# Performance work log

Measured on AMD Instinct MI355X. Metric: run time of the kernel, lower is better.

## Reference

```python
import jax, jax.numpy as jnp
import numpy as np

EPS = 1e-5

def _instance_norm(t):
    # torch .var(dim=2) default is unbiased (ddof=1) over flattened HW
    b, c, h, w = t.shape
    flat = t.reshape(b, c, h * w)
    mean = flat.mean(axis=2)
    var = flat.var(axis=2, ddof=1) + EPS
    return (t - mean[:, :, None, None]) / jnp.sqrt(var)[:, :, None, None]

def _conv1x1(t, w, b):
    # w: [Cout, Cin], b: [Cout]; t: [B, Cin, H, W]
    return jnp.einsum('oc,bchw->bohw', w, t) + b[None, :, None, None]


def setup_inputs() -> dict:
    key = jax.random.key(0)
    ks = jax.random.split(key, 11)
    B, C, H, W = 4, 512, 64, 64
    scale = 1.0 / np.sqrt(C)
    inp = {
        'c': jax.random.normal(ks[0], (B, C, H, W), jnp.float32),
        's': jax.random.normal(ks[1], (B, C, H, W), jnp.float32),
        'x': jax.random.normal(ks[2], (B, C, H, W), jnp.float32),
        'c_w': jax.random.normal(ks[3], (C, C), jnp.float32) * scale,
        'c_b': jax.random.normal(ks[4], (C,), jnp.float32) * 0.01,
        's_w': jax.random.normal(ks[5], (C, C), jnp.float32) * scale,
        's_b': jax.random.normal(ks[6], (C,), jnp.float32) * 0.01,
        'i_w': jax.random.normal(ks[7], (C, C), jnp.float32) * scale,
        'i_b': jax.random.normal(ks[8], (C,), jnp.float32) * 0.01,
        'o_w': jax.random.normal(ks[9], (C, C), jnp.float32) * scale,
        'o_b': jax.random.normal(ks[10], (C,), jnp.float32) * 0.01,
    }
    return inp


def reference(c, s, x, c_w, c_b, s_w, s_b, i_w, i_b, o_w, o_b):
    B, C, H, W = c.shape
    N = H * W
    cf = _conv1x1(_instance_norm(c), c_w, c_b).reshape(B, C, N)
    sf = _conv1x1(_instance_norm(s), s_w, s_b).reshape(B, C, N)
    xf = _conv1x1(s, i_w, i_b).reshape(B, C, N)
    # mask[b, n, m] = sum_c cf[b, c, n] * sf[b, c, m]; softmax over m
    mask = jax.nn.softmax(jnp.einsum('bcn,bcm->bnm', cf, sf), axis=-1)
    # of = xf @ mask^T : of[b, c, n] = sum_m xf[b, c, m] * mask[b, n, m]
    of = jnp.einsum('bcm,bnm->bcn', xf, mask).reshape(B, C, H, W)
    of = _conv1x1(of, o_w, o_b)
    return x + of
```

## Files before the change

kernel.cpp:

```cpp
#include <hip/hip_runtime.h>

typedef unsigned short u16;
typedef _Float16 f16x8 __attribute__((ext_vector_type(8)));
typedef float f32x4 __attribute__((ext_vector_type(4)));
typedef u16 u16x4 __attribute__((ext_vector_type(4)));
typedef u16 u16x8v __attribute__((ext_vector_type(8)));

__device__ __forceinline__ u16 f2h(float f) {
    _Float16 h = (_Float16)f;
    return __builtin_bit_cast(u16, h);
}
__device__ __forceinline__ float h2f(u16 u) {
    return (float)__builtin_bit_cast(_Float16, u);
}

__global__ void __launch_bounds__(256) stats_kernel(
    const float* __restrict__ c, const float* __restrict__ s,
    float* __restrict__ mC, float* __restrict__ rC,
    float* __restrict__ mS, float* __restrict__ rS)
{
    const float* src = (blockIdx.y ? s : c) + (size_t)blockIdx.x * 4096;
    int t = threadIdx.x, lane = t & 63, wv = t >> 6;
    const float4* p = (const float4*)src;
    float sum = 0.f, sq = 0.f;
#pragma unroll
    for (int i = 0; i < 4; ++i) {
        float4 v = p[t + 256 * i];
        sum += v.x + v.y + v.z + v.w;
        sq  += v.x * v.x + v.y * v.y + v.z * v.z + v.w * v.w;
    }
#pragma unroll
    for (int m = 1; m < 64; m <<= 1) {
        sum += __shfl_xor(sum, m);
        sq  += __shfl_xor(sq, m);
    }
    __shared__ float sa[4], sb[4];
    if (!lane) { sa[wv] = sum; sb[wv] = sq; }
    __syncthreads();
    if (t == 0) {
        float S = sa[0] + sa[1] + sa[2] + sa[3];
        float Q = sb[0] + sb[1] + sb[2] + sb[3];
        float mean = S * (1.0f / 4096.0f);
        float var = (Q - 4096.0f * mean * mean) * (1.0f / 4095.0f);
        float rstd = rsqrtf(var + 1e-5f);
        if (blockIdx.y) { mS[blockIdx.x] = mean; rS[blockIdx.x] = rstd; }
        else            { mC[blockIdx.x] = mean; rC[blockIdx.x] = rstd; }
    }
}

__global__ void __launch_bounds__(256) packall(
    const float* __restrict__ c, const float* __restrict__ s,
    const float* __restrict__ mC, const float* __restrict__ rC,
    const float* __restrict__ mS, const float* __restrict__ rS,
    u16* __restrict__ cnT, u16* __restrict__ snT, u16* __restrict__ sRT)
{
    __shared__ float tile[32][33];
    int z = blockIdx.z;
    bool isS = z >= 4;
    int b = isS ? z - 4 : z;
    const float* src  = isS ? s : c;
    const float* mean = isS ? mS : mC;
    const float* rstd = isS ? rS : rC;
    u16* dh = isS ? snT : cnT;
    int n0 = blockIdx.x * 32, c0 = blockIdx.y * 32;
    int tx = threadIdx.x, ty = threadIdx.y;
    const float* sbp = src + ((size_t)b * 512 + c0) * 4096 + n0;
#pragma unroll
    for (int it = 0; it < 4; ++it) {
        int cc = ty + it * 8;
        tile[cc][tx] = sbp[(size_t)cc * 4096 + tx];
    }
    __syncthreads();
    int ch = c0 + tx;
    float mn = mean[b * 512 + ch];
    float rs = rstd[b * 512 + ch];
    size_t obase = ((size_t)b * 4096 + n0) * 512 + c0;
#pragma unroll
    for (int it = 0; it < 4; ++it) {
        int r = ty + it * 8;
        float v = tile[tx][r];
        size_t o = obase + (size_t)r * 512 + tx;
        dh[o] = f2h((v - mn) * rs);
        if (isS) sRT[o] = f2h(v);
    }
}

__global__ void __launch_bounds__(256) prep_kernel(
    const float* __restrict__ c_w, const float* __restrict__ s_w,
    const float* __restrict__ i_w, const float* __restrict__ o_w,
    u16* __restrict__ cwT, u16* __restrict__ swT,
    u16* __restrict__ iwT, u16* __restrict__ ow)
{
    int z = blockIdx.z;
    int tx = threadIdx.x, ty = threadIdx.y;
    if (z == 3) {
        size_t base = ((size_t)(blockIdx.y * 16 + blockIdx.x) * 256 +
                       (ty * 32 + tx)) * 4;
        float4 v = *(const float4*)(o_w + base);
        u16x4 o;
        o[0] = f2h(v.x); o[1] = f2h(v.y); o[2] = f2h(v.z); o[3] = f2h(v.w);
        *(u16x4*)(ow + base) = o;
        return;
    }
    const float* w = (z == 0) ? c_w : (z == 1) ? s_w : i_w;
    u16* wT = (z == 0) ? cwT : (z == 1) ? swT : iwT;
    __shared__ float tile[32][33];
    int c0 = blockIdx.x * 32, k0 = blockIdx.y * 32;
#pragma unroll
    for (int it = 0; it < 4; ++it) {
        int kk = ty + it * 8;
        tile[kk][tx] = w[(size_t)(k0 + kk) * 512 + c0 + tx];
    }
    __syncthreads();
#pragma unroll
    for (int it = 0; it < 4; ++it) {
        int r = ty + it * 8;
        wT[(size_t)(c0 + r) * 512 + k0 + tx] = f2h(tile[tx][r]);
    }
}

__global__ void __launch_bounds__(256) bias_prep(
    const float* __restrict__ o_w, const float* __restrict__ i_b,
    const float* __restrict__ o_b, const float* __restrict__ s_w,
    const float* __restrict__ c_b, float* __restrict__ v,
    float* __restrict__ wu)
{
    __shared__ float buf[512];
    int t = threadIdx.x;
    bool isWu = blockIdx.x >= 2;
    const float* vec = isWu ? c_b : i_b;
    buf[t] = vec[t]; buf[t + 256] = vec[t + 256];
    __syncthreads();
    int o = (blockIdx.x & 1) * 256 + t;
    if (!isWu) {
        float acc = o_b[o];
        const float* row = o_w + (size_t)o * 512;
        for (int k = 0; k < 512; ++k) acc += row[k] * buf[k];
        v[o] = acc;
    } else {
        float acc = 0.f;
        for (int k = 0; k < 512; ++k) acc += buf[k] * s_w[(size_t)k * 512 + o];
        wu[o] = acc;
    }
}

__global__ void __launch_bounds__(256) rowdot_kernel(
    const u16* __restrict__ snT, const float* __restrict__ wu,
    float* __restrict__ u)
{
    __shared__ float swu[512];
    int t = threadIdx.x;
    swu[t] = wu[t]; swu[t + 256] = wu[t + 256];
    __syncthreads();
    int lane = t & 63, wv = t >> 6;
    int row = blockIdx.x * 4 + wv;
    u16x8v h = *(const u16x8v*)(snT + (size_t)row * 512 + lane * 8);
    float acc = 0.f;
#pragma unroll
    for (int i = 0; i < 8; ++i) acc += h2f(h[i]) * swu[lane * 8 + i];
#pragma unroll
    for (int m = 1; m < 64; m <<= 1) acc += __shfl_xor(acc, m);
    if (!lane) u[row] = acc;
}

#define EPI_F32       0
#define EPI_PLAIN_F16 2

__device__ __forceinline__ void stageA(
    const u16* __restrict__ g, int ldk, int i0, int k0, char* tile, int wv, int lane)
{
#pragma unroll
    for (int cc = 0; cc < 4; ++cc) {
        int chunk = (wv * 4 + cc) * 64 + lane;
        int row  = chunk >> 3;
        int slot = chunk & 7;
        int gc   = slot ^ (row & 7);
        const u16* gp = g + (size_t)(i0 + row) * ldk + (k0 + gc * 8);
        char* lp = tile + (size_t)(wv * 4 + cc) * 1024;
        __builtin_amdgcn_global_load_lds(
            (const __attribute__((address_space(1))) unsigned int*)gp,
            (__attribute__((address_space(3))) unsigned int*)lp, 16, 0, 0);
    }
}
__device__ __forceinline__ void stageB(
    const u16* __restrict__ g, int ldk, int j0, int k0, char* tile, int wv, int lane)
{
#pragma unroll
    for (int cc = 0; cc < 2; ++cc) {
        int chunk = (wv * 2 + cc) * 64 + lane;
        int row  = chunk >> 3;
        int slot = chunk & 7;
        int gc   = slot ^ (row & 7);
        const u16* gp = g + (size_t)(j0 + row) * ldk + (k0 + gc * 8);
        char* lp = tile + (size_t)(wv * 2 + cc) * 1024;
        __builtin_amdgcn_global_load_lds(
            (const __attribute__((address_space(1))) unsigned int*)gp,
            (__attribute__((address_space(3))) unsigned int*)lp, 16, 0, 0);
    }
}

template<int EPI>
__global__ void __launch_bounds__(512) gemm_bt(
    const u16* __restrict__ A_, const u16* __restrict__ B_,
    int K, int ldk, const float* __restrict__ bias,
    const float* __restrict__ jb, long jbZ,
    float* __restrict__ outF_, u16* __restrict__ outH_,
    int ldo, int zdiv,
    long aBatch, long aChunk, long bBatch, long bChunk, long oZ)
{
    __shared__ char smem[49152];

    int bz = blockIdx.z;
    int batch = bz / zdiv, chunk = bz % zdiv;
    const u16* A  = A_ + (size_t)batch * aBatch + (size_t)chunk * aChunk;
    const u16* Bm = B_ + (size_t)batch * bBatch + (size_t)chunk * bChunk;

    int i0 = blockIdx.y * 256, j0 = blockIdx.x * 128;
    int tid = threadIdx.x, lane = tid & 63, wv = tid >> 6;
    int wr = wv >> 1, wc = wv & 1;
    int r15 = lane & 15, h4 = lane >> 4;

    f32x4 zero = {0.f, 0.f, 0.f, 0.f};
    f32x4 acc[4][4];
#pragma unroll
    for (int m = 0; m < 4; ++m)
#pragma unroll
        for (int n = 0; n < 4; ++n) acc[m][n] = zero;

    for (int k0 = 0; k0 < K; k0 += 64) {
        stageA(A, ldk, i0, k0, smem, wv, lane);
        stageB(Bm, ldk, j0, k0, smem + 32768, wv, lane);
        asm volatile("s_waitcnt vmcnt(0)" ::: "memory");
        __syncthreads();
#pragma unroll
        for (int ks = 0; ks < 2; ++ks) {
            f16x8 a[4], b[4];
#pragma unroll
            for (int m = 0; m < 4; ++m) {
                int row = wr * 64 + m * 16 + r15;
                int off = row * 128 + (((ks * 4 + h4) ^ (row & 7)) << 4);
                a[m] = *(const f16x8*)(smem + off);
            }
#pragma unroll
            for (int n = 0; n < 4; ++n) {
                int col = wc * 64 + n * 16 + r15;
                int off = col * 128 + (((ks * 4 + h4) ^ (col & 7)) << 4);
                b[n] = *(const f16x8*)(smem + 32768 + off);
            }
#pragma unroll
            for (int m = 0; m < 4; ++m)
#pragma unroll
                for (int n = 0; n < 4; ++n)
                    acc[m][n] = __builtin_amdgcn_mfma_f32_16x16x32_f16(a[m], b[n], acc[m][n], 0, 0, 0);
        }
        __syncthreads();
    }

    float* outF = outF_ ? outF_ + (size_t)bz * oZ : nullptr;
    u16* outH = outH_ ? outH_ + (size_t)bz * oZ : nullptr;
    const float* jbp = jb ? jb + (size_t)bz * jbZ : nullptr;

#pragma unroll
    for (int m = 0; m < 4; ++m)
#pragma unroll
        for (int n = 0; n < 4; ++n) {
            int ibase = i0 + wr * 64 + m * 16 + h4 * 4;
            int j = j0 + wc * 64 + n * 16 + r15;
#pragma unroll
            for (int r = 0; r < 4; ++r) {
                int i = ibase + r;
                float v = acc[m][n][r];
                if constexpr (EPI == EPI_PLAIN_F16) {
                    if (bias) v += bias[i];
                    if (jbp) v += jbp[j];
                    outH[(size_t)i * ldo + j] = f2h(v);
                } else {
                    outF[(size_t)i * ldo + j] = v;
                }
            }
        }
}

__device__ __forceinline__ void stage256(
    const u16* __restrict__ g, int r0, int k0, char* tile, int wv, int lane)
{
#pragma unroll
    for (int cc = 0; cc < 4; ++cc) {
        int grp = cc * 8 + wv;
        int chunk = grp * 64 + lane;
        int row  = chunk >> 3;
        int slot = chunk & 7;
        int gc   = slot ^ (row & 7);
        const u16* gp = g + (size_t)(r0 + row) * 512 + (k0 + gc * 8);
        char* lp = tile + (size_t)grp * 1024;
        __builtin_amdgcn_global_load_lds(
            (const __attribute__((address_space(1))) unsigned int*)gp,
            (__attribute__((address_space(3))) unsigned int*)lp, 16, 0, 0);
    }
}

__global__ void __launch_bounds__(512) glogits256(
    const u16* __restrict__ A_, const u16* __restrict__ B_,
    const float* __restrict__ jb_, u16* __restrict__ outH_,
    long aZ, long bZ, long jbZ, long oZ)
{
    extern __shared__ char smem[];

    int bz = blockIdx.z;
    const u16* A  = A_ + (size_t)bz * aZ;
    const u16* Bm = B_ + (size_t)bz * bZ;

    int i0 = blockIdx.y * 256, j0 = blockIdx.x * 256;
    int tid = threadIdx.x, lane = tid & 63, wv = tid >> 6;
    int wr = wv >> 2, wc = wv & 3;
    int r15 = lane & 15, h4 = lane >> 4;

    f32x4 zero = {0.f, 0.f, 0.f, 0.f};
    f32x4 acc[8][4];
#pragma unroll
    for (int m = 0; m < 8; ++m)
#pragma unroll
        for (int n = 0; n < 4; ++n) acc[m][n] = zero;

    for (int k0 = 0; k0 < 512; k0 += 64) {
        stage256(A,  i0, k0, smem,         wv, lane);
        stage256(Bm, j0, k0, smem + 32768, wv, lane);
        asm volatile("s_waitcnt vmcnt(0)" ::: "memory");
        __syncthreads();
#pragma unroll
        for (int ks = 0; ks < 2; ++ks) {
            f16x8 a[8], b[4];
#pragma unroll
            for (int m = 0; m < 8; ++m) {
                int row = wr * 128 + m * 16 + r15;
                int off = row * 128 + (((ks * 4 + h4) ^ (row & 7)) << 4);
                a[m] = *(const f16x8*)(smem + off);
            }
#pragma unroll
            for (int n = 0; n < 4; ++n) {
                int col = wc * 64 + n * 16 + r15;
                int off = col * 128 + (((ks * 4 + h4) ^ (col & 7)) << 4);
                b[n] = *(const f16x8*)(smem + 32768 + off);
            }
#pragma unroll
            for (int m = 0; m < 8; ++m)
#pragma unroll
                for (int n = 0; n < 4; ++n)
                    acc[m][n] = __builtin_amdgcn_mfma_f32_16x16x32_f16(a[m], b[n], acc[m][n], 0, 0, 0);
        }
        __syncthreads();
    }

    u16* outH = outH_ + (size_t)bz * oZ;
    const float* jbp = jb_ + (size_t)bz * jbZ;
#pragma unroll
    for (int m = 0; m < 8; ++m)
#pragma unroll
        for (int n = 0; n < 4; ++n) {
            int ibase = i0 + wr * 128 + m * 16 + h4 * 4;
            int j = j0 + wc * 64 + n * 16 + r15;
            float ub = jbp[j];
#pragma unroll
            for (int r = 0; r < 4; ++r) {
                int i = ibase + r;
                outH[(size_t)i * 4096 + j] = f2h(acc[m][n][r] + ub);
            }
        }
}

__global__ void __launch_bounds__(256) softmax16(u16* __restrict__ LP)
{
    u16x8v* row = (u16x8v*)(LP + (size_t)blockIdx.x * 4096);
    int t = threadIdx.x, lane = t & 63, wv = t >> 6;
    u16x8v ca = row[t], cb = row[t + 256];
    float va[8], vb[8];
    float mx = -3.4e38f;
#pragma unroll
    for (int i = 0; i < 8; ++i) {
        va[i] = h2f(ca[i]); vb[i] = h2f(cb[i]);
        mx = fmaxf(mx, fmaxf(va[i], vb[i]));
    }
#pragma unroll
    for (int m = 1; m < 64; m <<= 1) mx = fmaxf(mx, __shfl_xor(mx, m));
    __shared__ float sM[4], sS[4];
    if (!lane) sM[wv] = mx;
    __syncthreads();
    mx = fmaxf(fmaxf(sM[0], sM[1]), fmaxf(sM[2], sM[3]));
    float sum = 0.f;
#pragma unroll
    for (int i = 0; i < 8; ++i) {
        va[i] = __expf(va[i] - mx);
        vb[i] = __expf(vb[i] - mx);
        sum += va[i] + vb[i];
    }
#pragma unroll
    for (int m = 1; m < 64; m <<= 1) sum += __shfl_xor(sum, m);
    if (!lane) sS[wv] = sum;
    __syncthreads();
    sum = sS[0] + sS[1] + sS[2] + sS[3];
    float inv = 1.0f / sum;
    u16x8v oa, ob;
#pragma unroll
    for (int i = 0; i < 8; ++i) {
        oa[i] = f2h(va[i] * inv);
        ob[i] = f2h(vb[i] * inv);
    }
    row[t] = oa; row[t + 256] = ob;
}

__global__ void __launch_bounds__(256) reduce4resid(
    const u16* __restrict__ part, const float* __restrict__ xr,
    const float* __restrict__ v, float* __restrict__ out)
{
    const size_t PLANE = 2097152;
    int b = blockIdx.y;
    size_t g8 = ((size_t)blockIdx.x * 256 + threadIdx.x) * 8;
    const u16* p0 = part + (size_t)b * 4 * PLANE + g8;
    float acc[8] = {0.f, 0.f, 0.f, 0.f, 0.f, 0.f, 0.f, 0.f};
#pragma unroll
    for (int k = 0; k < 4; ++k) {
        u16x8v h = *(const u16x8v*)(p0 + (size_t)k * PLANE);
#pragma unroll
        for (int i = 0; i < 8; ++i) acc[i] += h2f(h[i]);
    }
    const float4* xv = (const float4*)(xr + (size_t)b * PLANE + g8);
    float4 x0 = xv[0], x1 = xv[1];
    float vc = v[g8 >> 12];
    float4 o0, o1;
    o0.x = acc[0] + x0.x + vc; o0.y = acc[1] + x0.y + vc;
    o0.z = acc[2] + x0.z + vc; o0.w = acc[3] + x0.w + vc;
    o1.x = acc[4] + x1.x + vc; o1.y = acc[5] + x1.y + vc;
    o1.z = acc[6] + x1.z + vc; o1.w = acc[7] + x1.w + vc;
    float4* op = (float4*)(out + (size_t)b * PLANE + g8);
    op[0] = o0; op[1] = o1;
}

extern "C" void kernel_launch(void* const* d_in, const int* in_sizes, int n_in,
                              void* d_out, int out_size, void* d_ws, size_t ws_size,
                              hipStream_t stream)
{
    const float* c   = (const float*)d_in[0];
    const float* s   = (const float*)d_in[1];
    const float* x   = (const float*)d_in[2];
    const float* c_w = (const float*)d_in[3];
    const float* c_b = (const float*)d_in[4];
    const float* s_w = (const float*)d_in[5];
    const float* s_b = (const float*)d_in[6];
    const float* i_w = (const float*)d_in[7];
    const float* i_b = (const float*)d_in[8];
    const float* o_w = (const float*)d_in[9];
    const float* o_b = (const float*)d_in[10];
    float* out = (float*)d_out;
    char* ws = (char*)d_ws;

    const int B = 4, C = 512, N = 4096;
    const size_t NC = (size_t)N * C;
    const size_t W2 = (size_t)C * C;
    const size_t NN = (size_t)N * N;
    const int SMEM256 = 65536;

    size_t off = 0;
    auto alloc = [&](size_t bytes) { size_t o = off; off += (bytes + 255) & ~(size_t)255; return o; };

    size_t o_meanC = alloc((size_t)B * C * 4);
    size_t o_rstdC = alloc((size_t)B * C * 4);
    size_t o_meanS = alloc((size_t)B * C * 4);
    size_t o_rstdS = alloc((size_t)B * C * 4);
    size_t o_cwT = alloc(W2 * 2);
    size_t o_swT = alloc(W2 * 2);
    size_t o_iwT = alloc(W2 * 2);
    size_t o_ow  = alloc(W2 * 2);
    size_t o_G   = alloc(W2 * 2);
    size_t o_W   = alloc(W2 * 2);
    size_t o_v   = alloc((size_t)C * 4);
    size_t o_wu  = alloc((size_t)C * 4);
    size_t o_u   = alloc((size_t)B * N * 4);
    size_t o_cnT = alloc(B * NC * 2);
    size_t o_snT = alloc(B * NC * 2);
    size_t o_sRT = alloc(B * NC * 2);
    size_t o_sgT = alloc(B * NC * 2);
    size_t o_sW  = alloc(B * NC * 2);
    size_t o_P   = alloc(2 * NN * 2);
    size_t o_pt  = alloc(8 * NC * 2);

    if (ws_size < off) {
        (void)hipMemsetAsync(d_out, 0, (size_t)out_size * 4, stream);
        return;
    }

    float* meanC = (float*)(ws + o_meanC);
    float* rstdC = (float*)(ws + o_rstdC);
    float* meanS = (float*)(ws + o_meanS);
    float* rstdS = (float*)(ws + o_rstdS);
    u16* cwT = (u16*)(ws + o_cwT);
    u16* swT = (u16*)(ws + o_swT);
    u16* iwT = (u16*)(ws + o_iwT);
    u16* ow  = (u16*)(ws + o_ow);
    u16* Gf  = (u16*)(ws + o_G);
    u16* Wf  = (u16*)(ws + o_W);
    float* vb = (float*)(ws + o_v);
    float* wu = (float*)(ws + o_wu);
    float* ub = (float*)(ws + o_u);
    u16* cnT = (u16*)(ws + o_cnT);
    u16* snT = (u16*)(ws + o_snT);
    u16* sRT = (u16*)(ws + o_sRT);
    u16* sgT = (u16*)(ws + o_sgT);
    u16* sW  = (u16*)(ws + o_sW);
    u16* Pb  = (u16*)(ws + o_P);
    u16* partH = (u16*)(ws + o_pt);

    stats_kernel<<<dim3(B * C, 2), 256, 0, stream>>>(c, s, meanC, rstdC, meanS, rstdS);
    packall<<<dim3(N / 32, C / 32, 8), dim3(32, 8), 0, stream>>>(
        c, s, meanC, rstdC, meanS, rstdS, cnT, snT, sRT);
    prep_kernel<<<dim3(16, 16, 4), dim3(32, 8), 0, stream>>>(
        c_w, s_w, i_w, o_w, cwT, swT, iwT, ow);
    bias_prep<<<dim3(4), 256, 0, stream>>>(o_w, i_b, o_b, s_w, c_b, vb, wu);
    gemm_bt<EPI_PLAIN_F16><<<dim3(4, 2, 2), 512, 0, stream>>>(
        cwT, swT, 512, 512, nullptr, nullptr, 0, nullptr, Gf, 512, 1,
        (long)(3 * W2), 0, (long)W2, 0, (long)W2);
    gemm_bt<EPI_PLAIN_F16><<<dim3(4, 16, B), 512, 0, stream>>>(
        snT, Gf, 512, 512, nullptr, nullptr, 0, nullptr, sgT, 512, 1,
        (long)NC, 0, 0, 0, (long)NC);
    gemm_bt<EPI_PLAIN_F16><<<dim3(32, 2, B), 512, 0, stream>>>(
        Wf, sRT, 512, 512, nullptr, nullptr, 0, nullptr, sW, 4096, 1,
        0, 0, (long)NC, 0, (long)NC);
    rowdot_kernel<<<dim3(B * N / 4), 256, 0, stream>>>(snT, wu, ub);
    for (int pb0 = 0; pb0 < B; pb0 += 2) {
        glogits256<<<dim3(16, 16, 2), 512, SMEM256, stream>>>(
            cnT + (size_t)pb0 * NC, sgT + (size_t)pb0 * NC,
            ub + (size_t)pb0 * N, Pb,
            (long)NC, (long)NC, (long)N, (long)NN);
        softmax16<<<dim3(2 * N), 256, 0, stream>>>(Pb);
        gemm_bt<EPI_PLAIN_F16><<<dim3(32, 2, 8), 512, 0, stream>>>(
            sW + (size_t)pb0 * NC, Pb, 1024, 4096, nullptr, nullptr, 0,
            nullptr, partH, 4096, 4,
            (long)NC, 1024L, (long)NN, 1024L, (long)NC);
        reduce4resid<<<dim3((int)(NC / 2048), 2), 256, 0, stream>>>(
            partH, x + (size_t)pb0 * NC, vb, out + (size_t)pb0 * NC);
    }
}
```

Measured before the change: 339.8 us.

## Fold instance-norm into the G matrix and fuse stats into the transpose pack

The separate stats pass over c and s is removed. Per-tile partial sums are now computed inside the transpose/pack kernel and reduced by a small statreduce kernel, and c and s are packed raw to f16 instead of normalized. The normalization is moved algebraically into a per-batch scaled G matrix (rC·G·rS) and a per-batch bias vector for the rowdot term, which also removes the duplicate sRT buffer. This saves one full read of c and s plus one f16 write, at the cost of extra small kernels and per-batch G copies. Dropping the mean subtraction on c should cancel under softmax, but relying on an unnormalized f16 path and E[x²]-mean² variance risks some precision loss.

```diff
diff --git a/kernel.cpp b/kernel.cpp
--- a/kernel.cpp
+++ b/kernel.cpp
@@ -14,54 +14,17 @@
     return (float)__builtin_bit_cast(_Float16, u);
 }
 
-__global__ void __launch_bounds__(256) stats_kernel(
+__global__ void __launch_bounds__(256) packstat(
     const float* __restrict__ c, const float* __restrict__ s,
-    float* __restrict__ mC, float* __restrict__ rC,
-    float* __restrict__ mS, float* __restrict__ rS)
-{
-    const float* src = (blockIdx.y ? s : c) + (size_t)blockIdx.x * 4096;
-    int t = threadIdx.x, lane = t & 63, wv = t >> 6;
-    const float4* p = (const float4*)src;
-    float sum = 0.f, sq = 0.f;
-#pragma unroll
-    for (int i = 0; i < 4; ++i) {
-        float4 v = p[t + 256 * i];
-        sum += v.x + v.y + v.z + v.w;
-        sq  += v.x * v.x + v.y * v.y + v.z * v.z + v.w * v.w;
-    }
-#pragma unroll
-    for (int m = 1; m < 64; m <<= 1) {
-        sum += __shfl_xor(sum, m);
-        sq  += __shfl_xor(sq, m);
-    }
-    __shared__ float sa[4], sb[4];
-    if (!lane) { sa[wv] = sum; sb[wv] = sq; }
-    __syncthreads();
-    if (t == 0) {
-        float S = sa[0] + sa[1] + sa[2] + sa[3];
-        float Q = sb[0] + sb[1] + sb[2] + sb[3];
-        float mean = S * (1.0f / 4096.0f);
-        float var = (Q - 4096.0f * mean * mean) * (1.0f / 4095.0f);
-        float rstd = rsqrtf(var + 1e-5f);
-        if (blockIdx.y) { mS[blockIdx.x] = mean; rS[blockIdx.x] = rstd; }
-        else            { mC[blockIdx.x] = mean; rC[blockIdx.x] = rstd; }
-    }
-}
-
-__global__ void __launch_bounds__(256) packall(
-    const float* __restrict__ c, const float* __restrict__ s,
-    const float* __restrict__ mC, const float* __restrict__ rC,
-    const float* __restrict__ mS, const float* __restrict__ rS,
-    u16* __restrict__ cnT, u16* __restrict__ snT, u16* __restrict__ sRT)
+    u16* __restrict__ cT, u16* __restrict__ sT,
+    float* __restrict__ pS, float* __restrict__ pQ)
 {
     __shared__ float tile[32][33];
     int z = blockIdx.z;
     bool isS = z >= 4;
-    int b = isS ? z - 4 : z;
-    const float* src  = isS ? s : c;
-    const float* mean = isS ? mS : mC;
-    const float* rstd = isS ? rS : rC;
-    u16* dh = isS ? snT : cnT;
+    int b = z & 3;
+    const float* src = isS ? s : c;
+    u16* dst = isS ? sT : cT;
     int n0 = blockIdx.x * 32, c0 = blockIdx.y * 32;
     int tx = threadIdx.x, ty = threadIdx.y;
     const float* sbp = src + ((size_t)b * 512 + c0) * 4096 + n0;
@@ -71,17 +34,48 @@
         tile[cc][tx] = sbp[(size_t)cc * 4096 + tx];
     }
     __syncthreads();
-    int ch = c0 + tx;
-    float mn = mean[b * 512 + ch];
-    float rs = rstd[b * 512 + ch];
     size_t obase = ((size_t)b * 4096 + n0) * 512 + c0;
 #pragma unroll
     for (int it = 0; it < 4; ++it) {
         int r = ty + it * 8;
-        float v = tile[tx][r];
-        size_t o = obase + (size_t)r * 512 + tx;
-        dh[o] = f2h((v - mn) * rs);
-        if (isS) sRT[o] = f2h(v);
+        dst[obase + (size_t)r * 512 + tx] = f2h(tile[tx][r]);
+    }
+    if (ty == 0) {
+        float sm = 0.f, sq = 0.f;
+#pragma unroll
+        for (int n = 0; n < 32; ++n) {
+            float v = tile[tx][n];
+            sm += v; sq += v * v;
+        }
+        size_t idx = ((size_t)z * 512 + c0 + tx) * 128 + blockIdx.x;
+        pS[idx] = sm; pQ[idx] = sq;
+    }
+}
+
+__global__ void __launch_bounds__(64) statreduce(
+    const float* __restrict__ pS, const float* __restrict__ pQ,
+    float* __restrict__ mC, float* __restrict__ rC,
+    float* __restrict__ mS, float* __restrict__ rS)
+{
+    int row = blockIdx.x;
+    int lane = threadIdx.x;
+    const float* ps = pS + (size_t)row * 128;
+    const float* pq = pQ + (size_t)row * 128;
+    float sm = ps[lane] + ps[lane + 64];
+    float sq = pq[lane] + pq[lane + 64];
+#pragma unroll
+    for (int m = 1; m < 64; m <<= 1) {
+        sm += __shfl_xor(sm, m);
+        sq += __shfl_xor(sq, m);
+    }
+    if (lane == 0) {
+        float mean = sm * (1.0f / 4096.0f);
+        float var = (sq - 4096.0f * mean * mean) * (1.0f / 4095.0f);
+        float rstd = rsqrtf(var + 1e-5f);
+        int z = row >> 9, ch = row & 511;
+        int b = z & 3;
+        if (z < 4) { mC[b * 512 + ch] = mean; rC[b * 512 + ch] = rstd; }
+        else       { mS[b * 512 + ch] = mean; rS[b * 512 + ch] = rstd; }
     }
 }
 
@@ -144,17 +138,54 @@
     }
 }
 
+__global__ void __launch_bounds__(256) wb_kernel(
+    const u16* __restrict__ G, const float* __restrict__ wu,
+    const float* __restrict__ mC, const float* __restrict__ rC,
+    const float* __restrict__ rS, float* __restrict__ wb)
+{
+    __shared__ float mr[512];
+    int b = blockIdx.y;
+    int t = threadIdx.x;
+    mr[t] = mC[b * 512 + t] * rC[b * 512 + t];
+    mr[t + 256] = mC[b * 512 + t + 256] * rC[b * 512 + t + 256];
+    __syncthreads();
+    int l = blockIdx.x * 256 + t;
+    float g = 0.f;
+    for (int a = 0; a < 512; ++a) g += mr[a] * h2f(G[(size_t)a * 512 + l]);
+    wb[b * 512 + l] = (wu[l] - g) * rS[b * 512 + l];
+}
+
+__global__ void __launch_bounds__(256) gbscale(
+    const u16* __restrict__ G, const float* __restrict__ rC,
+    const float* __restrict__ rS, u16* __restrict__ Gb)
+{
+    int b = blockIdx.y;
+    size_t idx = ((size_t)blockIdx.x * 256 + threadIdx.x) * 8;
+    int a = (int)(idx >> 9), l0 = (int)(idx & 511);
+    float ra = rC[b * 512 + a];
+    u16x8v g = *(const u16x8v*)(G + idx);
+    const float4* q4 = (const float4*)(rS + b * 512 + l0);
+    float4 q0 = q4[0], q1 = q4[1];
+    u16x8v o;
+    o[0] = f2h(ra * h2f(g[0]) * q0.x); o[1] = f2h(ra * h2f(g[1]) * q0.y);
+    o[2] = f2h(ra * h2f(g[2]) * q0.z); o[3] = f2h(ra * h2f(g[3]) * q0.w);
+    o[4] = f2h(ra * h2f(g[4]) * q1.x); o[5] = f2h(ra * h2f(g[5]) * q1.y);
+    o[6] = f2h(ra * h2f(g[6]) * q1.z); o[7] = f2h(ra * h2f(g[7]) * q1.w);
+    *(u16x8v*)(Gb + (size_t)b * 262144 + idx) = o;
+}
+
 __global__ void __launch_bounds__(256) rowdot_kernel(
-    const u16* __restrict__ snT, const float* __restrict__ wu,
+    const u16* __restrict__ sT, const float* __restrict__ wb,
     float* __restrict__ u)
 {
     __shared__ float swu[512];
     int t = threadIdx.x;
-    swu[t] = wu[t]; swu[t + 256] = wu[t + 256];
+    const float* wbb = wb + (size_t)(blockIdx.x >> 10) * 512;
+    swu[t] = wbb[t]; swu[t + 256] = wbb[t + 256];
     __syncthreads();
     int lane = t & 63, wv = t >> 6;
     int row = blockIdx.x * 4 + wv;
-    u16x8v h = *(const u16x8v*)(snT + (size_t)row * 512 + lane * 8);
+    u16x8v h = *(const u16x8v*)(sT + (size_t)row * 512 + lane * 8);
     float acc = 0.f;
 #pragma unroll
     for (int i = 0; i < 8; ++i) acc += h2f(h[i]) * swu[lane * 8 + i];
@@ -472,12 +503,15 @@
     size_t o_ow  = alloc(W2 * 2);
     size_t o_G   = alloc(W2 * 2);
     size_t o_W   = alloc(W2 * 2);
+    size_t o_Gb  = alloc((size_t)B * W2 * 2);
     size_t o_v   = alloc((size_t)C * 4);
     size_t o_wu  = alloc((size_t)C * 4);
+    size_t o_wb  = alloc((size_t)B * C * 4);
     size_t o_u   = alloc((size_t)B * N * 4);
-    size_t o_cnT = alloc(B * NC * 2);
-    size_t o_snT = alloc(B * NC * 2);
-    size_t o_sRT = alloc(B * NC * 2);
+    size_t o_pS  = alloc((size_t)8 * 512 * 128 * 4);
+    size_t o_pQ  = alloc((size_t)8 * 512 * 128 * 4);
+    size_t o_cT  = alloc(B * NC * 2);
+    size_t o_sT  = alloc(B * NC * 2);
     size_t o_sgT = alloc(B * NC * 2);
     size_t o_sW  = alloc(B * NC * 2);
     size_t o_P   = alloc(2 * NN * 2);
@@ -498,36 +532,41 @@
     u16* ow  = (u16*)(ws + o_ow);
     u16* Gf  = (u16*)(ws + o_G);
     u16* Wf  = (u16*)(ws + o_W);
+    u16* Gb  = (u16*)(ws + o_Gb);
     float* vb = (float*)(ws + o_v);
     float* wu = (float*)(ws + o_wu);
+    float* wb = (float*)(ws + o_wb);
     float* ub = (float*)(ws + o_u);
-    u16* cnT = (u16*)(ws + o_cnT);
-    u16* snT = (u16*)(ws + o_snT);
-    u16* sRT = (u16*)(ws + o_sRT);
+    float* pS = (float*)(ws + o_pS);
+    float* pQ = (float*)(ws + o_pQ);
+    u16* cT  = (u16*)(ws + o_cT);
+    u16* sT  = (u16*)(ws + o_sT);
     u16* sgT = (u16*)(ws + o_sgT);
     u16* sW  = (u16*)(ws + o_sW);
     u16* Pb  = (u16*)(ws + o_P);
     u16* partH = (u16*)(ws + o_pt);
 
-    stats_kernel<<<dim3(B * C, 2), 256, 0, stream>>>(c, s, meanC, rstdC, meanS, rstdS);
-    packall<<<dim3(N / 32, C / 32, 8), dim3(32, 8), 0, stream>>>(
-        c, s, meanC, rstdC, meanS, rstdS, cnT, snT, sRT);
+    packstat<<<dim3(N / 32, C / 32, 8), dim3(32, 8), 0, stream>>>(
+        c, s, cT, sT, pS, pQ);
+    statreduce<<<dim3(8 * 512), 64, 0, stream>>>(pS, pQ, meanC, rstdC, meanS, rstdS);
     prep_kernel<<<dim3(16, 16, 4), dim3(32, 8), 0, stream>>>(
         c_w, s_w, i_w, o_w, cwT, swT, iwT, ow);
     bias_prep<<<dim3(4), 256, 0, stream>>>(o_w, i_b, o_b, s_w, c_b, vb, wu);
     gemm_bt<EPI_PLAIN_F16><<<dim3(4, 2, 2), 512, 0, stream>>>(
         cwT, swT, 512, 512, nullptr, nullptr, 0, nullptr, Gf, 512, 1,
         (long)(3 * W2), 0, (long)W2, 0, (long)W2);
+    wb_kernel<<<dim3(2, B), 256, 0, stream>>>(Gf, wu, meanC, rstdC, rstdS, wb);
+    gbscale<<<dim3(128, B), 256, 0, stream>>>(Gf, rstdC, rstdS, Gb);
     gemm_bt<EPI_PLAIN_F16><<<dim3(4, 16, B), 512, 0, stream>>>(
-        snT, Gf, 512, 512, nullptr, nullptr, 0, nullptr, sgT, 512, 1,
-        (long)NC, 0, 0, 0, (long)NC);
+        sT, Gb, 512, 512, nullptr, nullptr, 0, nullptr, sgT, 512, 1,
+        (long)NC, 0, (long)W2, 0, (long)NC);
     gemm_bt<EPI_PLAIN_F16><<<dim3(32, 2, B), 512, 0, stream>>>(
-        Wf, sRT, 512, 512, nullptr, nullptr, 0, nullptr, sW, 4096, 1,
+        Wf, sT, 512, 512, nullptr, nullptr, 0, nullptr, sW, 4096, 1,
         0, 0, (long)NC, 0, (long)NC);
-    rowdot_kernel<<<dim3(B * N / 4), 256, 0, stream>>>(snT, wu, ub);
+    rowdot_kernel<<<dim3(B * N / 4), 256, 0, stream>>>(sT, wb, ub);
     for (int pb0 = 0; pb0 < B; pb0 += 2) {
         glogits256<<<dim3(16, 16, 2), 512, SMEM256, stream>>>(
-            cnT + (size_t)pb0 * NC, sgT + (size_t)pb0 * NC,
+            cT + (size_t)pb0 * NC, sgT + (size_t)pb0 * NC,
             ub + (size_t)pb0 * N, Pb,
             (long)NC, (long)NC, (long)N, (long)NN);
         softmax16<<<dim3(2 * N), 256, 0, stream>>>(Pb);
```

Measured after the change: 355.2 us. 1.05x slower.
